# Kernel optimization log

Measured on AMD Instinct MI355X. Metric: run time of the kernel, lower is better.

## Reference

```python
import jax, jax.numpy as jnp
import numpy as np

B, T, C = 4, 2048, 1024
E, H, K = 8, 2048, 2


def setup_inputs() -> dict:
    key = jax.random.key(0)
    ks = jax.random.split(key, 7)
    s_in = 1.0 / np.sqrt(C)
    s_hid = 1.0 / np.sqrt(H)
    return {
        "x": jax.random.normal(ks[0], (B, T, C), dtype=jnp.float32),
        "gate_w": jax.random.uniform(ks[1], (C, E), jnp.float32, -s_in, s_in),
        "gate_b": jnp.zeros((E,), jnp.float32),
        "w1": jax.random.uniform(ks[2], (E, C, H), jnp.float32, -s_in, s_in),
        "b1": jax.random.uniform(ks[3], (E, H), jnp.float32, -s_in, s_in),
        "w2": jax.random.uniform(ks[4], (E, H, C), jnp.float32, -s_hid, s_hid),
        "b2": jax.random.uniform(ks[5], (E, C), jnp.float32, -s_hid, s_hid),
    }


def reference(x, gate_w, gate_b, w1, b1, w2, b2):
    b, t, c = x.shape
    xf = x.reshape(b * t, c)  # (N, C)

    # TopKGate: softmax over expert logits, take top-k gate values/indices
    logits = xf @ gate_w + gate_b              # (N, E)
    probs = jax.nn.softmax(logits, axis=-1)
    gates, expert_idx = jax.lax.top_k(probs, K)  # (N, K) each

    # Dense all-experts MLP (faithful to the original which runs every expert)
    h = jax.nn.relu(jnp.einsum('nc,ech->neh', xf, w1) + b1)  # (N, E, H)
    expert_out = jnp.einsum('neh,ehc->nec', h, w2) + b2      # (N, E, C)

    # Combine weights: scatter top-k gate values into (N, E), then weighted sum
    onehot = jax.nn.one_hot(expert_idx, E, dtype=xf.dtype)   # (N, K, E)
    weights = jnp.einsum('nk,nke->ne', gates, onehot)        # (N, E)
    out = jnp.einsum('ne,nec->nc', weights, expert_out)      # (N, C)
    return out.reshape(b, t, c)
```

## Files before the change

kernel.cpp:

```cpp
#include <hip/hip_runtime.h>
#include <cstdint>
#include <cstddef>

typedef __attribute__((ext_vector_type(8))) short short8;
typedef __attribute__((ext_vector_type(4))) float f32x4;
typedef __attribute__((ext_vector_type(4))) float flt4;

#define DEV __device__ __forceinline__

constexpr int C_ = 1024, E_ = 8, H_ = 2048, K_TOP = 2;
constexpr int N_ = 8192;
constexpr int NK_ = N_ * K_TOP;
constexpr int HB_ = 32;

DEV unsigned short f2bf(float f){
  unsigned u = __float_as_uint(f);
  u += 0x7fffu + ((u >> 16) & 1u);
  return (unsigned short)(u >> 16);
}

DEV void gload16(const void* g, void* l){
  __builtin_amdgcn_global_load_lds((const __attribute__((address_space(1))) unsigned int*)g,
                                   (__attribute__((address_space(3))) unsigned int*)l,
                                   16, 0, 0);
}

__global__ void cvt_x_kernel(const float* __restrict__ s, unsigned short* __restrict__ d){
  size_t i = ((size_t)blockIdx.x * blockDim.x + threadIdx.x) * 8;
  flt4 v0 = *(const flt4*)(s + i);
  flt4 v1 = *(const flt4*)(s + i + 4);
  short8 o;
  o[0]=f2bf(v0[0]); o[1]=f2bf(v0[1]); o[2]=f2bf(v0[2]); o[3]=f2bf(v0[3]);
  o[4]=f2bf(v1[0]); o[5]=f2bf(v1[1]); o[6]=f2bf(v1[2]); o[7]=f2bf(v1[3]);
  *(short8*)(d + i) = o;
}

__global__ void tconv_kernel(const float* __restrict__ src, unsigned short* __restrict__ dst,
                             int R, int S){
  __shared__ float tile[32][33];
  int e = blockIdx.z;
  int r0 = blockIdx.y * 32, s0 = blockIdx.x * 32;
  const float* se = src + (size_t)e * R * S;
  unsigned short* de = dst + (size_t)e * R * S;
  int tx = threadIdx.x & 31, ty = threadIdx.x >> 5;
  #pragma unroll
  for (int i = 0; i < 4; i++){
    int r = ty + i * 8;
    tile[r][tx] = se[(size_t)(r0 + r) * S + s0 + tx];
  }
  __syncthreads();
  #pragma unroll
  for (int i = 0; i < 4; i++){
    int s = ty + i * 8;
    de[(size_t)(s0 + s) * R + r0 + tx] = f2bf(tile[tx][s]);
  }
}

__global__ void gate_kernel(const float* __restrict__ x, const float* __restrict__ gw,
                            const float* __restrict__ gb,
                            int* __restrict__ tok_e, float* __restrict__ tok_g){
  int lane = threadIdx.x & 63;
  int n = blockIdx.x * 4 + (threadIdx.x >> 6);
  const float* xr = x + (size_t)n * C_;
  float acc[E_];
  #pragma unroll
  for (int e = 0; e < E_; e++) acc[e] = 0.f;
  #pragma unroll 4
  for (int j = 0; j < C_ / 64; j++){
    int c = lane + j * 64;
    float xv = xr[c];
    flt4 g0 = *(const flt4*)(gw + (size_t)c * E_);
    flt4 g1 = *(const flt4*)(gw + (size_t)c * E_ + 4);
    acc[0] += xv * g0[0]; acc[1] += xv * g0[1]; acc[2] += xv * g0[2]; acc[3] += xv * g0[3];
    acc[4] += xv * g1[0]; acc[5] += xv * g1[1]; acc[6] += xv * g1[2]; acc[7] += xv * g1[3];
  }
  #pragma unroll
  for (int e = 0; e < E_; e++)
    #pragma unroll
    for (int off = 32; off > 0; off >>= 1)
      acc[e] += __shfl_xor(acc[e], off, 64);
  if (lane == 0){
    float l[E_], p[E_];
    float m = -1e30f;
    #pragma unroll
    for (int e = 0; e < E_; e++){ l[e] = acc[e] + gb[e]; m = fmaxf(m, l[e]); }
    float s = 0.f;
    #pragma unroll
    for (int e = 0; e < E_; e++){ p[e] = expf(l[e] - m); s += p[e]; }
    float inv = 1.f / s;
    int e0 = 0; float m0 = p[0];
    #pragma unroll
    for (int e = 1; e < E_; e++) if (p[e] > m0){ m0 = p[e]; e0 = e; }
    int e1 = -1; float m1 = -1.f;
    #pragma unroll
    for (int e = 0; e < E_; e++) if (e != e0 && p[e] > m1){ m1 = p[e]; e1 = e; }
    tok_e[2*n]   = e0; tok_g[2*n]   = m0 * inv;
    tok_e[2*n+1] = e1; tok_g[2*n+1] = m1 * inv;
  }
}

__global__ void hist_kernel(const int* __restrict__ tok_e, int* __restrict__ blockhist){
  __shared__ int h[E_];
  if (threadIdx.x < E_) h[threadIdx.x] = 0;
  __syncthreads();
  int n = blockIdx.x * 256 + threadIdx.x;
  int e0 = tok_e[2*n], e1 = tok_e[2*n+1];
  atomicAdd(&h[e0], 1);
  atomicAdd(&h[e1], 1);
  __syncthreads();
  if (threadIdx.x < E_) blockhist[blockIdx.x * E_ + threadIdx.x] = h[threadIdx.x];
}

__global__ void scan2_kernel(const int* __restrict__ blockhist, int* __restrict__ counts,
                             int* __restrict__ offsets, int* __restrict__ blockbase){
  if (threadIdx.x == 0){
    int tot[E_];
    for (int e = 0; e < E_; e++){
      int s = 0;
      for (int b = 0; b < HB_; b++) s += blockhist[b * E_ + e];
      tot[e] = s;
    }
    int s = 0;
    for (int e = 0; e < E_; e++){ counts[e] = tot[e]; offsets[e] = s; s += tot[e]; }
    for (int e = 0; e < E_; e++){
      int cur = offsets[e];
      for (int b = 0; b < HB_; b++){ blockbase[b * E_ + e] = cur; cur += blockhist[b * E_ + e]; }
    }
  }
}

__global__ void build_kernel(const int* __restrict__ tok_e, const float* __restrict__ tok_g,
                             const int* __restrict__ blockbase,
                             int* __restrict__ list_tok, float* __restrict__ list_gate){
  __shared__ int cur[E_];
  if (threadIdx.x < E_) cur[threadIdx.x] = blockbase[blockIdx.x * E_ + threadIdx.x];
  __syncthreads();
  int n = blockIdx.x * 256 + threadIdx.x;
  #pragma unroll
  for (int k = 0; k < K_TOP; k++){
    int e = tok_e[2*n + k];
    int pos = atomicAdd(&cur[e], 1);
    list_tok[pos] = n;
    list_gate[pos] = tok_g[2*n + k];
  }
}

template<bool FIRST>
__global__ __launch_bounds__(256, 2)
void moe_gemm(const unsigned short* __restrict__ Abase,
              const unsigned short* __restrict__ Bbase,
              const float* __restrict__ bias,
              const int* __restrict__ counts, const int* __restrict__ offsets,
              const int* __restrict__ list_tok, const float* __restrict__ list_gate,
              unsigned short* __restrict__ hbuf, float* __restrict__ out){
  constexpr int K   = FIRST ? C_ : H_;
  constexpr int ND  = FIRST ? H_ : C_;
  constexpr int GX  = ND / 128;
  constexpr int LGX = FIRST ? 4 : 3;
  constexpr int GY  = N_ / 256;
  __shared__ unsigned char smem[49152];

  int lin  = blockIdx.x + GX * (blockIdx.y + GY * blockIdx.z);
  int work = (lin & 7) * (GX * GY) + (lin >> 3);
  int bx = work & (GX - 1);
  int by = (work >> LGX) & (GY - 1);
  int e  = work >> (LGX + 5);

  int ne = counts[e];
  int row0 = by * 256;
  if (row0 >= ne) return;
  int off = offsets[e];
  int col0 = bx * 128;
  int tid = threadIdx.x;
  int lane = tid & 63, wave = tid >> 6;
  int wm = wave >> 1, wn = wave & 1;
  int lr = lane & 15, lk = lane >> 4;

  int rr = tid >> 3;
  int chunk = (tid & 7) ^ (rr & 7);
  const unsigned short* Bexp = Bbase + (size_t)e * ND * K;
  const unsigned short* agsrc[8];
  #pragma unroll
  for (int j = 0; j < 8; j++){
    int rc = min(row0 + j * 32 + rr, ne - 1);
    size_t arow = FIRST ? (size_t)list_tok[off + rc] * C_ : (size_t)(off + rc) * H_;
    agsrc[j] = Abase + arow + chunk * 8;
  }
  const unsigned short* bgsrc[4];
  #pragma unroll
  for (int j = 0; j < 4; j++)
    bgsrc[j] = Bexp + (size_t)(col0 + j * 32 + rr) * K + chunk * 8;
  unsigned char* Ad = smem + wave * 1024;
  unsigned char* Bd = smem + 32768 + wave * 1024;

  f32x4 acc[8][4];
  #pragma unroll
  for (int a = 0; a < 8; a++)
    #pragma unroll
    for (int b = 0; b < 4; b++) acc[a][b] = (f32x4){0.f,0.f,0.f,0.f};

  for (int k0 = 0; k0 < K; k0 += 64){
    __syncthreads();
    #pragma unroll
    for (int j = 0; j < 8; j++) gload16(agsrc[j] + k0, Ad + j * 4096);
    #pragma unroll
    for (int j = 0; j < 4; j++) gload16(bgsrc[j] + k0, Bd + j * 4096);
    __syncthreads();
    #pragma unroll
    for (int s = 0; s < 2; s++){
      short8 av[8], bv[4];
      int kx = ((s * 4 + lk) ^ (lr & 7)) * 16;
      #pragma unroll
      for (int m = 0; m < 8; m++)
        av[m] = *(const short8*)(smem + (wm * 128 + m * 16 + lr) * 128 + kx);
      #pragma unroll
      for (int n = 0; n < 4; n++)
        bv[n] = *(const short8*)(smem + 32768 + (wn * 64 + n * 16 + lr) * 128 + kx);
      #pragma unroll
      for (int m = 0; m < 8; m++)
        #pragma unroll
        for (int n = 0; n < 4; n++)
          acc[m][n] = __builtin_amdgcn_mfma_f32_16x16x32_bf16(av[m], bv[n], acc[m][n], 0, 0, 0);
    }
  }

  if (FIRST){
    #pragma unroll
    for (int m = 0; m < 8; m++){
      int rbase = row0 + wm*128 + m*16 + lk*4;
      #pragma unroll
      for (int n = 0; n < 4; n++){
        int colb = col0 + wn*64 + n*16 + lr;
        float bv2 = bias[e*ND + colb];
        #pragma unroll
        for (int i = 0; i < 4; i++){
          int r = rbase + i;
          if (r < ne){
            float v = acc[m][n][i] + bv2;
            v = v > 0.f ? v : 0.f;
            hbuf[(size_t)(off + r)*H_ + colb] = f2bf(v);
          }
        }
      }
    }
  } else {
    #pragma unroll
    for (int m = 0; m < 8; m++){
      int rbase = row0 + wm*128 + m*16 + lk*4;
      #pragma unroll
      for (int i = 0; i < 4; i++){
        int r = rbase + i;
        if (r < ne){
          int pos = off + r;
          int tok = list_tok[pos];
          float g = list_gate[pos];
          float* orow = out + (size_t)tok * C_;
          #pragma unroll
          for (int n = 0; n < 4; n++){
            int colb = col0 + wn*64 + n*16 + lr;
            float v = (acc[m][n][i] + bias[e*ND + colb]) * g;
            atomicAdd(orow + colb, v);
          }
        }
      }
    }
  }
}

extern "C" void kernel_launch(void* const* d_in, const int* in_sizes, int n_in,
                              void* d_out, int out_size, void* d_ws, size_t ws_size,
                              hipStream_t stream){
  const float* x  = (const float*)d_in[0];
  const float* gw = (const float*)d_in[1];
  const float* gb = (const float*)d_in[2];
  const float* w1 = (const float*)d_in[3];
  const float* b1 = (const float*)d_in[4];
  const float* w2 = (const float*)d_in[5];
  const float* b2 = (const float*)d_in[6];
  float* out = (float*)d_out;

  char* p = (char*)d_ws;
  unsigned short* xb   = (unsigned short*)p; p += (size_t)N_*C_*2;
  unsigned short* w1t  = (unsigned short*)p; p += (size_t)E_*C_*H_*2;
  unsigned short* w2t  = (unsigned short*)p; p += (size_t)E_*C_*H_*2;
  unsigned short* hbuf = (unsigned short*)p; p += (size_t)NK_*H_*2;
  int*   tok_e     = (int*)p;   p += (size_t)NK_*4;
  float* tok_g     = (float*)p; p += (size_t)NK_*4;
  int*   list_tok  = (int*)p;   p += (size_t)NK_*4;
  float* list_gate = (float*)p; p += (size_t)NK_*4;
  int*   counts    = (int*)p;   p += 256;
  int*   offsets   = (int*)p;   p += 256;
  int*   blockhist = (int*)p;   p += HB_*E_*4;
  int*   blockbase = (int*)p;   p += HB_*E_*4;

  hipMemsetAsync(out, 0, (size_t)out_size * sizeof(float), stream);

  cvt_x_kernel<<<(N_*C_/8)/256, 256, 0, stream>>>(x, xb);
  tconv_kernel<<<dim3(H_/32, C_/32, E_), 256, 0, stream>>>(w1, w1t, C_, H_);
  tconv_kernel<<<dim3(C_/32, H_/32, E_), 256, 0, stream>>>(w2, w2t, H_, C_);
  gate_kernel<<<N_/4, 256, 0, stream>>>(x, gw, gb, tok_e, tok_g);
  hist_kernel<<<HB_, 256, 0, stream>>>(tok_e, blockhist);
  scan2_kernel<<<1, 64, 0, stream>>>(blockhist, counts, offsets, blockbase);
  build_kernel<<<HB_, 256, 0, stream>>>(tok_e, tok_g, blockbase, list_tok, list_gate);

  moe_gemm<true ><<<dim3(H_/128, N_/256, E_), 256, 0, stream>>>(xb,   w1t, b1, counts, offsets, list_tok, list_gate, hbuf, out);
  moe_gemm<false><<<dim3(C_/128, N_/256, E_), 256, 0, stream>>>(hbuf, w2t, b2, counts, offsets, list_tok, list_gate, hbuf, out);
}
```

Baseline: 395.6 us.

## Enlarge MoE GEMM tiles to 256x256 with 512 threads and split-K second GEMM

```diff
diff --git a/kernel.cpp b/kernel.cpp
--- a/kernel.cpp
+++ b/kernel.cpp
@@ -146,65 +146,69 @@
 }
 
 template<bool FIRST>
-__global__ __launch_bounds__(256, 2)
+__global__ __launch_bounds__(512, 4)
 void moe_gemm(const unsigned short* __restrict__ Abase,
               const unsigned short* __restrict__ Bbase,
               const float* __restrict__ bias,
               const int* __restrict__ counts, const int* __restrict__ offsets,
               const int* __restrict__ list_tok, const float* __restrict__ list_gate,
               unsigned short* __restrict__ hbuf, float* __restrict__ out){
-  constexpr int K   = FIRST ? C_ : H_;
-  constexpr int ND  = FIRST ? H_ : C_;
-  constexpr int GX  = ND / 128;
-  constexpr int LGX = FIRST ? 4 : 3;
-  constexpr int GY  = N_ / 256;
-  __shared__ unsigned char smem[49152];
-
-  int lin  = blockIdx.x + GX * (blockIdx.y + GY * blockIdx.z);
-  int work = (lin & 7) * (GX * GY) + (lin >> 3);
-  int bx = work & (GX - 1);
-  int by = (work >> LGX) & (GY - 1);
-  int e  = work >> (LGX + 5);
+  constexpr int K    = FIRST ? C_ : H_;
+  constexpr int Ksub = 1024;
+  constexpr int NT   = Ksub / 64;
+  constexpr int ND   = FIRST ? H_ : C_;
+  constexpr int GX   = FIRST ? 8 : 4;
+  __shared__ unsigned char smem[65536];
+
+  int lin  = blockIdx.x + GX * (blockIdx.y + 32 * blockIdx.z);
+  int work = (lin & 7) * 256 + (lin >> 3);
+  int bx, by, e, ks;
+  if (FIRST){
+    bx = work & 7; by = (work >> 3) & 31; e = work >> 8; ks = 0;
+  } else {
+    bx = work & 3; by = (work >> 2) & 31; int rem = work >> 7; e = rem >> 1; ks = rem & 1;
+  }
 
   int ne = counts[e];
   int row0 = by * 256;
   if (row0 >= ne) return;
   int off = offsets[e];
-  int col0 = bx * 128;
+  int col0 = bx * 256;
   int tid = threadIdx.x;
   int lane = tid & 63, wave = tid >> 6;
-  int wm = wave >> 1, wn = wave & 1;
+  int wm = wave >> 2, wn = wave & 3;
   int lr = lane & 15, lk = lane >> 4;
-
   int rr = tid >> 3;
   int chunk = (tid & 7) ^ (rr & 7);
+
   const unsigned short* Bexp = Bbase + (size_t)e * ND * K;
-  const unsigned short* agsrc[8];
-  #pragma unroll
-  for (int j = 0; j < 8; j++){
-    int rc = min(row0 + j * 32 + rr, ne - 1);
+  const unsigned short* agsrc[4];
+  const unsigned short* bgsrc[4];
+  #pragma unroll
+  for (int j = 0; j < 4; j++){
+    int r = j * 64 + rr;
+    int rc = min(row0 + r, ne - 1);
     size_t arow = FIRST ? (size_t)list_tok[off + rc] * C_ : (size_t)(off + rc) * H_;
-    agsrc[j] = Abase + arow + chunk * 8;
-  }
-  const unsigned short* bgsrc[4];
-  #pragma unroll
-  for (int j = 0; j < 4; j++)
-    bgsrc[j] = Bexp + (size_t)(col0 + j * 32 + rr) * K + chunk * 8;
+    agsrc[j] = Abase + arow + ks * Ksub + chunk * 8;
+    bgsrc[j] = Bexp + (size_t)(col0 + r) * K + ks * Ksub + chunk * 8;
+  }
+
+  f32x4 acc[8][4];
+  #pragma unroll
+  for (int a = 0; a < 8; a++)
+    #pragma unroll
+    for (int b = 0; b < 4; b++) acc[a][b] = (f32x4){0.f,0.f,0.f,0.f};
+
   unsigned char* Ad = smem + wave * 1024;
   unsigned char* Bd = smem + 32768 + wave * 1024;
 
-  f32x4 acc[8][4];
-  #pragma unroll
-  for (int a = 0; a < 8; a++)
-    #pragma unroll
-    for (int b = 0; b < 4; b++) acc[a][b] = (f32x4){0.f,0.f,0.f,0.f};
-
-  for (int k0 = 0; k0 < K; k0 += 64){
+  for (int t = 0; t < NT; ++t){
+    int k0 = t * 64;
     __syncthreads();
     #pragma unroll
-    for (int j = 0; j < 8; j++) gload16(agsrc[j] + k0, Ad + j * 4096);
-    #pragma unroll
-    for (int j = 0; j < 4; j++) gload16(bgsrc[j] + k0, Bd + j * 4096);
+    for (int j = 0; j < 4; j++) gload16(agsrc[j] + k0, Ad + j * 8192);
+    #pragma unroll
+    for (int j = 0; j < 4; j++) gload16(bgsrc[j] + k0, Bd + j * 8192);
     __syncthreads();
     #pragma unroll
     for (int s = 0; s < 2; s++){
@@ -258,7 +262,8 @@
           #pragma unroll
           for (int n = 0; n < 4; n++){
             int colb = col0 + wn*64 + n*16 + lr;
-            float v = (acc[m][n][i] + bias[e*ND + colb]) * g;
+            float bterm = ks == 0 ? bias[e*ND + colb] : 0.f;
+            float v = (acc[m][n][i] + bterm) * g;
             atomicAdd(orow + colb, v);
           }
         }
@@ -303,6 +308,6 @@
   scan2_kernel<<<1, 64, 0, stream>>>(blockhist, counts, offsets, blockbase);
   build_kernel<<<HB_, 256, 0, stream>>>(tok_e, tok_g, blockbase, list_tok, list_gate);
 
-  moe_gemm<true ><<<dim3(H_/128, N_/256, E_), 256, 0, stream>>>(xb,   w1t, b1, counts, offsets, list_tok, list_gate, hbuf, out);
-  moe_gemm<false><<<dim3(C_/128, N_/256, E_), 256, 0, stream>>>(hbuf, w2t, b2, counts, offsets, list_tok, list_gate, hbuf, out);
-}
+  moe_gemm<true ><<<dim3(8, 32, 8),  512, 0, stream>>>(xb,   w1t, b1, counts, offsets, list_tok, list_gate, hbuf, out);
+  moe_gemm<false><<<dim3(4, 32, 16), 512, 0, stream>>>(hbuf, w2t, b2, counts, offsets, list_tok, list_gate, hbuf, out);
+}
```

After: 1.213 ms. 3.07x slower.
